# Performance work log

Hardware: AMD Instinct MI355X
Metric: run time of the kernel (lower is better)

## Reference

```python
import jax, jax.numpy as jnp
import numpy as np

N = 50000
IN_C = 512
HID = 16
HEADS = 3
OUT_C = 128
NEG_SLOPE = 0.2


def _add_self_loops(edge_index, n):
    loop = jnp.arange(n, dtype=edge_index.dtype)
    src = jnp.concatenate([edge_index[0], loop])
    dst = jnp.concatenate([edge_index[1], loop])
    return src, dst


def gat_conv(x, W, a_src, a_dst, b, src, dst, n):
    # x: [N, Fin], W: [Fin, H*C], a_src/a_dst: [H, C], b: [H*C]
    H, C = a_src.shape
    h = (x @ W).reshape(n, H, C)                      # [N, H, C]
    e_src = jnp.einsum('nhc,hc->nh', h, a_src)        # [N, H]
    e_dst = jnp.einsum('nhc,hc->nh', h, a_dst)        # [N, H]
    e = jax.nn.leaky_relu(e_src[src] + e_dst[dst], NEG_SLOPE)  # [E, H]
    # segment softmax over incoming edges of each destination node
    m = jax.ops.segment_max(e, dst, num_segments=n)
    e = jnp.exp(e - m[dst])
    s = jax.ops.segment_sum(e, dst, num_segments=n)
    alpha = e / s[dst]                                 # [E, H]
    out = jax.ops.segment_sum(h[src] * alpha[:, :, None], dst, num_segments=n)
    return out.reshape(n, H * C) + b


def gcn_conv(x, W, b, src, dst, n):
    h = x @ W                                          # [N, Fout]
    ones = jnp.ones(src.shape[0], dtype=h.dtype)
    deg = jax.ops.segment_sum(ones, dst, num_segments=n)
    dinv = jax.lax.rsqrt(jnp.maximum(deg, 1.0))
    norm = dinv[src] * dinv[dst]                       # [E]
    out = jax.ops.segment_sum(h[src] * norm[:, None], dst, num_segments=n)
    return out + b


def setup_inputs() -> dict:
    key = jax.random.key(0)
    ks = jax.random.split(key, 16)
    E = 800000
    x = jax.random.normal(ks[0], (N, IN_C), dtype=jnp.float32)
    edge_index = jax.random.randint(ks[1], (2, E), 0, N, dtype=jnp.int64)

    def glorot(k, shape):
        fan = shape[0] + shape[-1]
        return jax.random.uniform(k, shape, jnp.float32, -1.0, 1.0) * np.sqrt(6.0 / fan)

    return {
        'x': x,
        'edge_index': edge_index,
        'W1': glorot(ks[2], (IN_C, HEADS * HID)),
        'a_src1': glorot(ks[3], (HEADS, HID)),
        'a_dst1': glorot(ks[4], (HEADS, HID)),
        'b1': jnp.zeros((HEADS * HID,), jnp.float32),
        'W2': glorot(ks[5], (HEADS * HID, OUT_C)),
        'a_src2': glorot(ks[6], (1, OUT_C)),
        'a_dst2': glorot(ks[7], (1, OUT_C)),
        'b2': jnp.zeros((OUT_C,), jnp.float32),
        'Wg': glorot(ks[8], (OUT_C, OUT_C)),
        'bg': jnp.zeros((OUT_C,), jnp.float32),
        'Wl': glorot(ks[9], (OUT_C, OUT_C)),
        'bl': jnp.zeros((OUT_C,), jnp.float32),
    }


def reference(x, edge_index, W1, a_src1, a_dst1, b1, W2, a_src2, a_dst2, b2, Wg, bg, Wl, bl):
    n = x.shape[0]
    src, dst = _add_self_loops(edge_index, n)
    # GATModel: gat1 (3 heads, concat) -> elu -> gat2 (1 head) -> log_softmax
    h = gat_conv(x, W1, a_src1, a_dst1, b1, src, dst, n)
    h = jax.nn.elu(h)
    h = gat_conv(h, W2, a_src2, a_dst2, b2, src, dst, n)
    h = jax.nn.log_softmax(h, axis=1)
    # GCN: only conv1 is used in its forward, followed by relu
    h = jax.nn.relu(gcn_conv(h, Wg, bg, src, dst, n))
    # Linear1
    return h @ Wl + bl
```

## Files before the change

kernel.cpp:

```cpp
#include <hip/hip_runtime.h>
#include <hip/hip_bf16.h>
#include <math.h>

#define NN 50000
#define EE 800000
#define ET 850000
#define NEG 0.2f

static __device__ __forceinline__ float lrelu(float x){ return x > 0.f ? x : NEG * x; }
static __device__ __forceinline__ void edge_sd(const int* __restrict__ ei, int e, int& s, int& d){
  if (e < EE){ s = ei[e]; d = ei[e + EE]; } else { s = e - EE; d = s; }
}

__global__ __launch_bounds__(256) void k_hist(const int* __restrict__ ei, int* __restrict__ deg_i)
{
  int e = blockIdx.x * 256 + threadIdx.x;
  if (e >= ET) return;
  int s, d; edge_sd(ei, e, s, d);
  atomicAdd(deg_i + d, 1);
}

__global__ __launch_bounds__(1024) void k_scan(const int* __restrict__ deg_i,
    int* __restrict__ row_start, float* __restrict__ dinv)
{
  __shared__ int bs[1024];
  int t = threadIdx.x;
  const int CH = (NN + 1023) / 1024;
  int base = t * CH;
  int sum = 0;
  for (int i = 0; i < CH; ++i){ int idx = base + i; if (idx < NN) sum += deg_i[idx]; }
  bs[t] = sum; __syncthreads();
  for (int off = 1; off < 1024; off <<= 1){
    int add = (t >= off) ? bs[t - off] : 0;
    __syncthreads();
    bs[t] += add;
    __syncthreads();
  }
  int run = (t == 0) ? 0 : bs[t - 1];
  for (int i = 0; i < CH; ++i){
    int idx = base + i;
    if (idx < NN){
      int dv = deg_i[idx];
      row_start[idx] = run;
      dinv[idx] = rsqrtf(fmaxf((float)dv, 1.0f));
      run += dv;
    }
  }
  if (t == 0) row_start[NN] = bs[1023];
}

__global__ __launch_bounds__(256) void k_fill(const int* __restrict__ ei,
    const int* __restrict__ row_start, int* __restrict__ cur, int* __restrict__ csr)
{
  int e = blockIdx.x * 256 + threadIdx.x;
  if (e >= ET) return;
  int s, d; edge_sd(ei, e, s, d);
  int pos = atomicAdd(cur + d, 1);
  csr[row_start[d] + pos] = s;
}

__global__ __launch_bounds__(256) void k_gat1_gemm(
    const float* __restrict__ x, const float* __restrict__ W1, float* __restrict__ h1)
{
  __shared__ float At[64][132];
  __shared__ float Bs[64][52];
  int t = threadIdx.x;
  int tx = t & 15, ty = t >> 4;
  int n0 = blockIdx.x * 128;
  float acc[8][3] = {};
  for (int kt = 0; kt < 512; kt += 64){
    __syncthreads();
#pragma unroll
    for (int p = 0; p < 8; ++p){
      int f = t + p * 256;
      int node = f >> 4, kq = f & 15;
      float4 v = make_float4(0.f, 0.f, 0.f, 0.f);
      int gn = n0 + node;
      if (gn < NN) v = *(const float4*)(x + (size_t)gn * 512 + kt + kq * 4);
      At[kq * 4 + 0][node] = v.x; At[kq * 4 + 1][node] = v.y;
      At[kq * 4 + 2][node] = v.z; At[kq * 4 + 3][node] = v.w;
    }
#pragma unroll
    for (int p = 0; p < 3; ++p){
      int f = t + p * 256;
      int k = f / 12, oq = f % 12;
      *(float4*)&Bs[k][oq * 4] = *(const float4*)(W1 + (size_t)(kt + k) * 48 + oq * 4);
    }
    __syncthreads();
#pragma unroll 4
    for (int k = 0; k < 64; ++k){
      float4 a0 = *(const float4*)&At[k][ty * 8];
      float4 a1 = *(const float4*)&At[k][ty * 8 + 4];
      float b0 = Bs[k][tx * 3 + 0], b1 = Bs[k][tx * 3 + 1], b2 = Bs[k][tx * 3 + 2];
      float av[8] = {a0.x, a0.y, a0.z, a0.w, a1.x, a1.y, a1.z, a1.w};
#pragma unroll
      for (int i = 0; i < 8; ++i){
        acc[i][0] = fmaf(av[i], b0, acc[i][0]);
        acc[i][1] = fmaf(av[i], b1, acc[i][1]);
        acc[i][2] = fmaf(av[i], b2, acc[i][2]);
      }
    }
  }
#pragma unroll
  for (int i = 0; i < 8; ++i){
    int gn = n0 + ty * 8 + i;
    if (gn < NN){
      float* o = h1 + (size_t)gn * 48 + tx * 3;
      o[0] = acc[i][0]; o[1] = acc[i][1]; o[2] = acc[i][2];
    }
  }
}

__global__ __launch_bounds__(256) void k_att1(const float* __restrict__ h1,
    const float* __restrict__ as1, const float* __restrict__ ad1,
    float* __restrict__ es1, float* __restrict__ ed1)
{
  int n = (blockIdx.x * 256 + threadIdx.x) >> 6;
  int lane = threadIdx.x & 63;
  if (n >= NN) return;
  float ps = 0.f, pd = 0.f;
  if (lane < 48){
    float v = h1[(size_t)n * 48 + lane];
    ps = v * as1[lane]; pd = v * ad1[lane];
  }
#pragma unroll
  for (int off = 8; off; off >>= 1){
    ps += __shfl_xor(ps, off, 16);
    pd += __shfl_xor(pd, off, 16);
  }
  if (lane < 48 && (lane & 15) == 0){
    es1[(size_t)n * 3 + (lane >> 4)] = ps;
    ed1[(size_t)n * 3 + (lane >> 4)] = pd;
  }
}

__global__ __launch_bounds__(256) void k_gat1_agg(
    const int* __restrict__ csr, const int* __restrict__ row_start,
    const float* __restrict__ es1, const float* __restrict__ ed1,
    const float* __restrict__ h1, const float* __restrict__ b1,
    float* __restrict__ o1)
{
  int dn = (blockIdx.x * 256 + threadIdx.x) >> 6;
  int lane = threadIdx.x & 63;
  if (dn >= NN) return;
  bool act = lane < 48;
  int hd = act ? (lane >> 4) : 0;
  int beg = row_start[dn], end = row_start[dn + 1];
  float edv = ed1[(size_t)dn * 3 + hd];
  float m = -INFINITY, sum = 0.f, acc = 0.f;
  int i = beg;
  for (; i + 1 < end; i += 2){
    int s0 = csr[i], s1 = csr[i + 1];
    float e0 = lrelu(es1[(size_t)s0 * 3 + hd] + edv);
    float e1 = lrelu(es1[(size_t)s1 * 3 + hd] + edv);
    float h0 = act ? h1[(size_t)s0 * 48 + lane] : 0.f;
    float h1v = act ? h1[(size_t)s1 * 48 + lane] : 0.f;
    float mn = fmaxf(m, fmaxf(e0, e1));
    float sc = __expf(m - mn), w0 = __expf(e0 - mn), w1 = __expf(e1 - mn);
    sum = sum * sc + w0 + w1;
    acc = acc * sc + h0 * w0 + h1v * w1;
    m = mn;
  }
  if (i < end){
    int s0 = csr[i];
    float e0 = lrelu(es1[(size_t)s0 * 3 + hd] + edv);
    float h0 = act ? h1[(size_t)s0 * 48 + lane] : 0.f;
    float mn = fmaxf(m, e0);
    float sc = __expf(m - mn), w0 = __expf(e0 - mn);
    sum = sum * sc + w0;
    acc = acc * sc + h0 * w0;
  }
  if (act){
    float v = acc / sum + b1[lane];
    o1[(size_t)dn * 48 + lane] = v > 0.f ? v : expm1f(v);
  }
}

__global__ __launch_bounds__(256) void k_gat2_gemm(const float* __restrict__ o1,
    const float* __restrict__ W2, const float* __restrict__ as2, const float* __restrict__ ad2,
    float* __restrict__ h2, float* __restrict__ es2, float* __restrict__ ed2)
{
  __shared__ float At[48][68];
  __shared__ float Ws[48][128];
  int t = threadIdx.x, tx = t & 15, ty = t >> 4;
  int n0 = blockIdx.x * 64;
#pragma unroll
  for (int p = 0; p < 3; ++p){
    int f = t + p * 256;
    int node = f / 12, kq = f % 12;
    float4 v = make_float4(0.f, 0.f, 0.f, 0.f);
    if (n0 + node < NN) v = *(const float4*)(o1 + (size_t)(n0 + node) * 48 + kq * 4);
    At[kq * 4 + 0][node] = v.x; At[kq * 4 + 1][node] = v.y;
    At[kq * 4 + 2][node] = v.z; At[kq * 4 + 3][node] = v.w;
  }
#pragma unroll
  for (int p = 0; p < 6; ++p){
    int f = t + p * 256;
    int k = f >> 5, cq = f & 31;
    *(float4*)&Ws[k][cq * 4] = *(const float4*)(W2 + (size_t)k * 128 + cq * 4);
  }
  __syncthreads();
  float acc[4][8] = {};
#pragma unroll 4
  for (int k = 0; k < 48; ++k){
    float4 a  = *(const float4*)&At[k][ty * 4];
    float4 c0 = *(const float4*)&Ws[k][tx * 4];
    float4 c1 = *(const float4*)&Ws[k][tx * 4 + 64];
    float av[4] = {a.x, a.y, a.z, a.w};
    float bv[8] = {c0.x, c0.y, c0.z, c0.w, c1.x, c1.y, c1.z, c1.w};
#pragma unroll
    for (int i = 0; i < 4; ++i)
#pragma unroll
      for (int j = 0; j < 8; ++j)
        acc[i][j] = fmaf(av[i], bv[j], acc[i][j]);
  }
  float asv[8], adv[8];
#pragma unroll
  for (int j = 0; j < 4; ++j){
    asv[j] = as2[tx * 4 + j];      asv[4 + j] = as2[64 + tx * 4 + j];
    adv[j] = ad2[tx * 4 + j];      adv[4 + j] = ad2[64 + tx * 4 + j];
  }
#pragma unroll
  for (int i = 0; i < 4; ++i){
    int gn = n0 + ty * 4 + i;
    float s = 0.f, d = 0.f;
#pragma unroll
    for (int j = 0; j < 8; ++j){ s = fmaf(acc[i][j], asv[j], s); d = fmaf(acc[i][j], adv[j], d); }
#pragma unroll
    for (int off = 1; off < 16; off <<= 1){
      s += __shfl_xor(s, off, 16);
      d += __shfl_xor(d, off, 16);
    }
    if (gn < NN){
      float4 o0 = make_float4(acc[i][0], acc[i][1], acc[i][2], acc[i][3]);
      float4 o1v = make_float4(acc[i][4], acc[i][5], acc[i][6], acc[i][7]);
      *(float4*)(h2 + (size_t)gn * 128 + tx * 4) = o0;
      *(float4*)(h2 + (size_t)gn * 128 + tx * 4 + 64) = o1v;
      if (tx == 0){ es2[gn] = s; ed2[gn] = d; }
    }
  }
}

__global__ __launch_bounds__(256) void k_gat2_agg(
    const int* __restrict__ csr, const int* __restrict__ row_start,
    const float* __restrict__ es2, const float* __restrict__ ed2,
    const float* __restrict__ h2, const float* __restrict__ b2,
    float* __restrict__ o2)
{
  int wid = (blockIdx.x * 256 + threadIdx.x) >> 6;
  int lane = threadIdx.x & 63;
  int half = lane >> 5, l32 = lane & 31;
  int d = wid * 2 + half;
  if (d >= NN) return;
  int beg = row_start[d], end = row_start[d + 1];
  float edv = ed2[d];
  float m = -INFINITY, sum = 0.f;
  float ax = 0.f, ay = 0.f, az = 0.f, aw = 0.f;
  int i = beg;
  for (; i + 1 < end; i += 2){
    int s0 = csr[i], s1 = csr[i + 1];
    float e0 = lrelu(es2[s0] + edv);
    float e1 = lrelu(es2[s1] + edv);
    float4 v0 = *(const float4*)(h2 + (size_t)s0 * 128 + l32 * 4);
    float4 v1 = *(const float4*)(h2 + (size_t)s1 * 128 + l32 * 4);
    float mn = fmaxf(m, fmaxf(e0, e1));
    float sc = __expf(m - mn), w0 = __expf(e0 - mn), w1 = __expf(e1 - mn);
    sum = sum * sc + w0 + w1;
    ax = ax * sc + v0.x * w0 + v1.x * w1;
    ay = ay * sc + v0.y * w0 + v1.y * w1;
    az = az * sc + v0.z * w0 + v1.z * w1;
    aw = aw * sc + v0.w * w0 + v1.w * w1;
    m = mn;
  }
  if (i < end){
    int s0 = csr[i];
    float e0 = lrelu(es2[s0] + edv);
    float4 v0 = *(const float4*)(h2 + (size_t)s0 * 128 + l32 * 4);
    float mn = fmaxf(m, e0);
    float sc = __expf(m - mn), w0 = __expf(e0 - mn);
    sum = sum * sc + w0;
    ax = ax * sc + v0.x * w0;
    ay = ay * sc + v0.y * w0;
    az = az * sc + v0.z * w0;
    aw = aw * sc + v0.w * w0;
  }
  float inv = 1.f / sum;
  float4 vb = *(const float4*)(b2 + l32 * 4);
  float v0 = ax * inv + vb.x, v1 = ay * inv + vb.y;
  float v2 = az * inv + vb.z, v3 = aw * inv + vb.w;
  float mx = fmaxf(fmaxf(v0, v1), fmaxf(v2, v3));
#pragma unroll
  for (int off = 16; off; off >>= 1) mx = fmaxf(mx, __shfl_xor(mx, off, 32));
  float es = __expf(v0 - mx) + __expf(v1 - mx) + __expf(v2 - mx) + __expf(v3 - mx);
#pragma unroll
  for (int off = 16; off; off >>= 1) es += __shfl_xor(es, off, 32);
  float lse = mx + __logf(es);
  float4 ov = make_float4(v0 - lse, v1 - lse, v2 - lse, v3 - lse);
  *(float4*)(o2 + (size_t)d * 128 + l32 * 4) = ov;
}

__global__ __launch_bounds__(256) void k_gcn_agg(
    const int* __restrict__ csr, const int* __restrict__ row_start,
    const float* __restrict__ dinv, const float* __restrict__ hg,
    float* __restrict__ og)
{
  int wid = (blockIdx.x * 256 + threadIdx.x) >> 6;
  int lane = threadIdx.x & 63;
  int half = lane >> 5, l32 = lane & 31;
  int d = wid * 2 + half;
  if (d >= NN) return;
  int beg = row_start[d], end = row_start[d + 1];
  float ax = 0.f, ay = 0.f, az = 0.f, aw = 0.f;
  float bx = 0.f, by = 0.f, bz = 0.f, bw = 0.f;
  int i = beg;
  for (; i + 1 < end; i += 2){
    int s0 = csr[i], s1 = csr[i + 1];
    float4 v0 = *(const float4*)(hg + (size_t)s0 * 128 + l32 * 4);
    float4 v1 = *(const float4*)(hg + (size_t)s1 * 128 + l32 * 4);
    ax += v0.x; ay += v0.y; az += v0.z; aw += v0.w;
    bx += v1.x; by += v1.y; bz += v1.z; bw += v1.w;
  }
  if (i < end){
    int s0 = csr[i];
    float4 v0 = *(const float4*)(hg + (size_t)s0 * 128 + l32 * 4);
    ax += v0.x; ay += v0.y; az += v0.z; aw += v0.w;
  }
  float dd = dinv[d];
  float4 ov = make_float4((ax + bx) * dd, (ay + by) * dd, (az + bz) * dd, (aw + bw) * dd);
  *(float4*)(og + (size_t)d * 128 + l32 * 4) = ov;
}

template<int PRE, int POST, int SCALE>
__global__ __launch_bounds__(256) void k_gemm128(const float* __restrict__ in,
    const float* __restrict__ W, const float* __restrict__ bpre,
    const float* __restrict__ bpost, const float* __restrict__ dinv,
    float* __restrict__ out)
{
  __shared__ float At[32][68];
  __shared__ float Ws[32][128];
  int t = threadIdx.x, tx = t & 15, ty = t >> 4;
  int n0 = blockIdx.x * 64;
  float acc[4][8] = {};
  for (int kt = 0; kt < 128; kt += 32){
    __syncthreads();
#pragma unroll
    for (int p = 0; p < 2; ++p){
      int f = t + p * 256;
      int node = f >> 3, kq = f & 7;
      float4 v = make_float4(0.f, 0.f, 0.f, 0.f);
      if (n0 + node < NN){
        v = *(const float4*)(in + (size_t)(n0 + node) * 128 + kt + kq * 4);
        if (PRE){
          const float* bp = bpre + kt + kq * 4;
          v.x = fmaxf(v.x + bp[0], 0.f); v.y = fmaxf(v.y + bp[1], 0.f);
          v.z = fmaxf(v.z + bp[2], 0.f); v.w = fmaxf(v.w + bp[3], 0.f);
        }
      }
      At[kq * 4 + 0][node] = v.x; At[kq * 4 + 1][node] = v.y;
      At[kq * 4 + 2][node] = v.z; At[kq * 4 + 3][node] = v.w;
    }
#pragma unroll
    for (int p = 0; p < 4; ++p){
      int f = t + p * 256;
      int k = f >> 5, cq = f & 31;
      *(float4*)&Ws[k][cq * 4] = *(const float4*)(W + (size_t)(kt + k) * 128 + cq * 4);
    }
    __syncthreads();
#pragma unroll 4
    for (int k = 0; k < 32; ++k){
      float4 a  = *(const float4*)&At[k][ty * 4];
      float4 c0 = *(const float4*)&Ws[k][tx * 4];
      float4 c1 = *(const float4*)&Ws[k][tx * 4 + 64];
      float av[4] = {a.x, a.y, a.z, a.w};
      float bv[8] = {c0.x, c0.y, c0.z, c0.w, c1.x, c1.y, c1.z, c1.w};
#pragma unroll
      for (int i = 0; i < 4; ++i)
#pragma unroll
        for (int j = 0; j < 8; ++j)
          acc[i][j] = fmaf(av[i], bv[j], acc[i][j]);
    }
  }
#pragma unroll
  for (int i = 0; i < 4; ++i){
    int gn = n0 + ty * 4 + i;
    if (gn < NN){
      float sc = SCALE ? dinv[gn] : 1.f;
      float4 o0, o1v;
      o0.x  = (acc[i][0] + (POST ? bpost[tx * 4 + 0] : 0.f)) * sc;
      o0.y  = (acc[i][1] + (POST ? bpost[tx * 4 + 1] : 0.f)) * sc;
      o0.z  = (acc[i][2] + (POST ? bpost[tx * 4 + 2] : 0.f)) * sc;
      o0.w  = (acc[i][3] + (POST ? bpost[tx * 4 + 3] : 0.f)) * sc;
      o1v.x = (acc[i][4] + (POST ? bpost[64 + tx * 4 + 0] : 0.f)) * sc;
      o1v.y = (acc[i][5] + (POST ? bpost[64 + tx * 4 + 1] : 0.f)) * sc;
      o1v.z = (acc[i][6] + (POST ? bpost[64 + tx * 4 + 2] : 0.f)) * sc;
      o1v.w = (acc[i][7] + (POST ? bpost[64 + tx * 4 + 3] : 0.f)) * sc;
      *(float4*)(out + (size_t)gn * 128 + tx * 4) = o0;
      *(float4*)(out + (size_t)gn * 128 + tx * 4 + 64) = o1v;
    }
  }
}

extern "C" void kernel_launch(void* const* d_in, const int* in_sizes, int n_in,
                              void* d_out, int out_size, void* d_ws, size_t ws_size,
                              hipStream_t stream)
{
  const float* x   = (const float*)d_in[0];
  const int*   ei  = (const int*)d_in[1];
  const float* W1  = (const float*)d_in[2];
  const float* as1 = (const float*)d_in[3];
  const float* ad1 = (const float*)d_in[4];
  const float* b1  = (const float*)d_in[5];
  const float* W2  = (const float*)d_in[6];
  const float* as2 = (const float*)d_in[7];
  const float* ad2 = (const float*)d_in[8];
  const float* b2  = (const float*)d_in[9];
  const float* Wg  = (const float*)d_in[10];
  const float* bg  = (const float*)d_in[11];
  const float* Wl  = (const float*)d_in[12];
  const float* bl  = (const float*)d_in[13];
  float* out = (float*)d_out;

  float* ws = (float*)d_ws;
  const size_t n = NN;
  float* h1   = ws;
  float* h2   = ws + 48 * n;
  float* o1   = ws + 176 * n;
  float* o2   = ws + 224 * n;
  float* es1  = ws + 352 * n;
  float* ed1  = ws + 355 * n;
  float* es2  = ws + 358 * n;
  float* ed2  = ws + 359 * n;
  float* dinv = ws + 360 * n;
  int* ints   = (int*)(ws + 361 * n);
  int* deg_i     = ints;
  int* cur       = ints + n;
  int* row_start = ints + 2 * n;
  int* csr       = ints + 3 * n + 1;
  float* og = o2;

  hipMemsetAsync(deg_i, 0, 2 * n * sizeof(int), stream);

  const int egrid = (ET + 255) / 256;
  const int wgrid = (NN * 64) / 256;
  const int hgrid = (NN / 2 * 64) / 256;
  k_hist<<<egrid, 256, 0, stream>>>(ei, deg_i);
  k_scan<<<1, 1024, 0, stream>>>(deg_i, row_start, dinv);
  k_fill<<<egrid, 256, 0, stream>>>(ei, row_start, cur, csr);
  k_gat1_gemm<<<(NN + 127) / 128, 256, 0, stream>>>(x, W1, h1);
  k_att1<<<wgrid, 256, 0, stream>>>(h1, as1, ad1, es1, ed1);
  k_gat1_agg<<<wgrid, 256, 0, stream>>>(csr, row_start, es1, ed1, h1, b1, o1);
  k_gat2_gemm<<<(NN + 63) / 64, 256, 0, stream>>>(o1, W2, as2, ad2, h2, es2, ed2);
  k_gat2_agg<<<hgrid, 256, 0, stream>>>(csr, row_start, es2, ed2, h2, b2, o2);
  k_gemm128<0, 0, 1><<<(NN + 63) / 64, 256, 0, stream>>>(o2, Wg, nullptr, nullptr, dinv, h2);
  k_gcn_agg<<<hgrid, 256, 0, stream>>>(csr, row_start, dinv, h2, og);
  k_gemm128<1, 1, 0><<<(NN + 63) / 64, 256, 0, stream>>>(og, Wl, bg, bl, nullptr, out);
}
```

Before: 683.6 us.

## Parallelize degree scan across blocks and fuse attention logits into GAT1 GEMM

Replaces the single-block 1024-thread prefix scan over node degrees with a three-kernel multi-block scan (per-block sums, top-level scan, final scan). It also computes the per-head source and destination attention logits in the GAT1 GEMM epilogue using 16-lane shuffles, which removes the separate k_att1 kernel and its re-read of h1. The cost is two extra tiny launches for the scan and some extra shuffle work in the GEMM epilogue.

```diff
diff --git a/kernel.cpp b/kernel.cpp
--- a/kernel.cpp
+++ b/kernel.cpp
@@ -5,6 +5,7 @@
 #define NN 50000
 #define EE 800000
 #define ET 850000
+#define NB 196
 #define NEG 0.2f
 
 static __device__ __forceinline__ float lrelu(float x){ return x > 0.f ? x : NEG * x; }
@@ -20,33 +21,56 @@
   atomicAdd(deg_i + d, 1);
 }
 
-__global__ __launch_bounds__(1024) void k_scan(const int* __restrict__ deg_i,
-    int* __restrict__ row_start, float* __restrict__ dinv)
-{
-  __shared__ int bs[1024];
+__global__ __launch_bounds__(256) void k_scan_part(const int* __restrict__ deg_i, int* __restrict__ bsum)
+{
+  __shared__ int wsum[4];
   int t = threadIdx.x;
-  const int CH = (NN + 1023) / 1024;
-  int base = t * CH;
-  int sum = 0;
-  for (int i = 0; i < CH; ++i){ int idx = base + i; if (idx < NN) sum += deg_i[idx]; }
-  bs[t] = sum; __syncthreads();
-  for (int off = 1; off < 1024; off <<= 1){
+  int i = blockIdx.x * 256 + t;
+  int v = (i < NN) ? deg_i[i] : 0;
+  int r = v;
+#pragma unroll
+  for (int off = 32; off; off >>= 1) r += __shfl_xor(r, off);
+  if ((t & 63) == 0) wsum[t >> 6] = r;
+  __syncthreads();
+  if (t == 0) bsum[blockIdx.x] = wsum[0] + wsum[1] + wsum[2] + wsum[3];
+}
+
+__global__ __launch_bounds__(256) void k_scan_top(const int* __restrict__ bsum, int* __restrict__ boff)
+{
+  __shared__ int bs[256];
+  int t = threadIdx.x;
+  int v = (t < NB) ? bsum[t] : 0;
+  bs[t] = v;
+  __syncthreads();
+  for (int off = 1; off < 256; off <<= 1){
     int add = (t >= off) ? bs[t - off] : 0;
     __syncthreads();
     bs[t] += add;
     __syncthreads();
   }
-  int run = (t == 0) ? 0 : bs[t - 1];
-  for (int i = 0; i < CH; ++i){
-    int idx = base + i;
-    if (idx < NN){
-      int dv = deg_i[idx];
-      row_start[idx] = run;
-      dinv[idx] = rsqrtf(fmaxf((float)dv, 1.0f));
-      run += dv;
-    }
-  }
-  if (t == 0) row_start[NN] = bs[1023];
+  if (t < NB) boff[t] = bs[t] - v;
+}
+
+__global__ __launch_bounds__(256) void k_scan_fin(const int* __restrict__ deg_i,
+    const int* __restrict__ boff, int* __restrict__ row_start, float* __restrict__ dinv)
+{
+  __shared__ int bs[256];
+  int t = threadIdx.x;
+  int i = blockIdx.x * 256 + t;
+  int v = (i < NN) ? deg_i[i] : 0;
+  bs[t] = v;
+  __syncthreads();
+  for (int off = 1; off < 256; off <<= 1){
+    int add = (t >= off) ? bs[t - off] : 0;
+    __syncthreads();
+    bs[t] += add;
+    __syncthreads();
+  }
+  if (i < NN){
+    row_start[i] = boff[blockIdx.x] + bs[t] - v;
+    dinv[i] = rsqrtf(fmaxf((float)v, 1.0f));
+  }
+  if (i == 0) row_start[NN] = ET;
 }
 
 __global__ __launch_bounds__(256) void k_fill(const int* __restrict__ ei,
@@ -60,7 +84,9 @@
 }
 
 __global__ __launch_bounds__(256) void k_gat1_gemm(
-    const float* __restrict__ x, const float* __restrict__ W1, float* __restrict__ h1)
+    const float* __restrict__ x, const float* __restrict__ W1,
+    const float* __restrict__ as1, const float* __restrict__ ad1,
+    float* __restrict__ h1, float* __restrict__ es1, float* __restrict__ ed1)
 {
   __shared__ float At[64][132];
   __shared__ float Bs[64][52];
@@ -104,33 +130,30 @@
 #pragma unroll
   for (int i = 0; i < 8; ++i){
     int gn = n0 + ty * 8 + i;
+    float ps0 = 0.f, ps1 = 0.f, ps2 = 0.f, pd0 = 0.f, pd1 = 0.f, pd2 = 0.f;
+#pragma unroll
+    for (int j = 0; j < 3; ++j){
+      int o = tx * 3 + j;
+      int h = o >> 4;
+      float a = acc[i][j];
+      float vs = a * as1[o], vd = a * ad1[o];
+      if (h == 0){ ps0 += vs; pd0 += vd; }
+      else if (h == 1){ ps1 += vs; pd1 += vd; }
+      else { ps2 += vs; pd2 += vd; }
+    }
+#pragma unroll
+    for (int off = 1; off < 16; off <<= 1){
+      ps0 += __shfl_xor(ps0, off, 16); ps1 += __shfl_xor(ps1, off, 16); ps2 += __shfl_xor(ps2, off, 16);
+      pd0 += __shfl_xor(pd0, off, 16); pd1 += __shfl_xor(pd1, off, 16); pd2 += __shfl_xor(pd2, off, 16);
+    }
     if (gn < NN){
       float* o = h1 + (size_t)gn * 48 + tx * 3;
       o[0] = acc[i][0]; o[1] = acc[i][1]; o[2] = acc[i][2];
-    }
-  }
-}
-
-__global__ __launch_bounds__(256) void k_att1(const float* __restrict__ h1,
-    const float* __restrict__ as1, const float* __restrict__ ad1,
-    float* __restrict__ es1, float* __restrict__ ed1)
-{
-  int n = (blockIdx.x * 256 + threadIdx.x) >> 6;
-  int lane = threadIdx.x & 63;
-  if (n >= NN) return;
-  float ps = 0.f, pd = 0.f;
-  if (lane < 48){
-    float v = h1[(size_t)n * 48 + lane];
-    ps = v * as1[lane]; pd = v * ad1[lane];
-  }
-#pragma unroll
-  for (int off = 8; off; off >>= 1){
-    ps += __shfl_xor(ps, off, 16);
-    pd += __shfl_xor(pd, off, 16);
-  }
-  if (lane < 48 && (lane & 15) == 0){
-    es1[(size_t)n * 3 + (lane >> 4)] = ps;
-    ed1[(size_t)n * 3 + (lane >> 4)] = pd;
+      if (tx == 0){
+        es1[(size_t)gn * 3 + 0] = ps0; es1[(size_t)gn * 3 + 1] = ps1; es1[(size_t)gn * 3 + 2] = ps2;
+        ed1[(size_t)gn * 3 + 0] = pd0; ed1[(size_t)gn * 3 + 1] = pd1; ed1[(size_t)gn * 3 + 2] = pd2;
+      }
+    }
   }
 }
 
@@ -436,6 +459,8 @@
   int* cur       = ints + n;
   int* row_start = ints + 2 * n;
   int* csr       = ints + 3 * n + 1;
+  int* bsum      = ints + 3 * n + 1 + ET;
+  int* boff      = ints + 3 * n + 1 + ET + NB;
   float* og = o2;
 
   hipMemsetAsync(deg_i, 0, 2 * n * sizeof(int), stream);
@@ -444,10 +469,11 @@
   const int wgrid = (NN * 64) / 256;
   const int hgrid = (NN / 2 * 64) / 256;
   k_hist<<<egrid, 256, 0, stream>>>(ei, deg_i);
-  k_scan<<<1, 1024, 0, stream>>>(deg_i, row_start, dinv);
+  k_scan_part<<<NB, 256, 0, stream>>>(deg_i, bsum);
+  k_scan_top<<<1, 256, 0, stream>>>(bsum, boff);
+  k_scan_fin<<<NB, 256, 0, stream>>>(deg_i, boff, row_start, dinv);
   k_fill<<<egrid, 256, 0, stream>>>(ei, row_start, cur, csr);
-  k_gat1_gemm<<<(NN + 127) / 128, 256, 0, stream>>>(x, W1, h1);
-  k_att1<<<wgrid, 256, 0, stream>>>(h1, as1, ad1, es1, ed1);
+  k_gat1_gemm<<<(NN + 127) / 128, 256, 0, stream>>>(x, W1, as1, ad1, h1, es1, ed1);
   k_gat1_agg<<<wgrid, 256, 0, stream>>>(csr, row_start, es1, ed1, h1, b1, o1);
   k_gat2_gemm<<<(NN + 63) / 64, 256, 0, stream>>>(o1, W2, as2, ad2, h2, es2, ed2);
   k_gat2_agg<<<hgrid, 256, 0, stream>>>(csr, row_start, es2, ed2, h2, b2, o2);
```

Measured after the change: 565.2 us. 1.21x faster.
